# Performance work log

Measured on AMD Instinct MI355X. Metric: run time of the kernel, lower is better.

## Reference

```python
import jax, jax.numpy as jnp
import numpy as np

B, K, N, D = 16384, 32, 100000, 256


def setup_inputs() -> dict:
    key = jax.random.key(0)
    k1, k2 = jax.random.split(key)
    neigh_ids = jax.random.randint(k1, (B, K), 0, N)  # neighbor node ids per batch node
    features = jax.random.normal(k2, (N, D), dtype=jnp.float32)  # node feature/embedding table
    return {"neigh_ids": neigh_ids, "features": features}


def reference(neigh_ids, features):
    # Original builds a normalized [B, U] mask and does mask @ features[unique_ids];
    # that is exactly a mean over each row's neighbor features. We compute it
    # directly via gather + mean, honoring the sparse structure.
    gathered = features[neigh_ids]            # [B, K, D]
    to_feats = jnp.mean(gathered, axis=1)     # mean aggregation (mask.div(num_neigh) @ embed)
    return jax.nn.relu(to_feats)              # [B, D]
```

## Files before the change

### kernel.cpp

```cpp
#include <hip/hip_runtime.h>


constexpr int K  = 32;
constexpr int D  = 256;
constexpr int D4 = D / 4;

__global__ __launch_bounds__(256) void gnn_agg_kernel(
    const int* __restrict__ neigh_ids,
    const float* __restrict__ features,
    float* __restrict__ out,
    int n_rows)
{
    const int waves_per_block = blockDim.x >> 6;
    const int lane = threadIdx.x & 63;
    const int row_stride = gridDim.x * waves_per_block;

    const float4* __restrict__ f4 = reinterpret_cast<const float4*>(features);
    float4* __restrict__ o4 = reinterpret_cast<float4*>(out);

    for (int row = blockIdx.x * waves_per_block + (threadIdx.x >> 6);
         row < n_rows; row += row_stride) {

        const int4* __restrict__ idp =
            reinterpret_cast<const int4*>(neigh_ids + (size_t)row * K);
        int4 id8[K / 4];
        #pragma unroll
        for (int c = 0; c < K / 4; ++c) id8[c] = idp[c];

        float4 acc = make_float4(0.f, 0.f, 0.f, 0.f);
        #pragma unroll
        for (int c = 0; c < K / 4; ++c) {
            const float4 v0 = f4[(size_t)id8[c].x * D4 + lane];
            const float4 v1 = f4[(size_t)id8[c].y * D4 + lane];
            const float4 v2 = f4[(size_t)id8[c].z * D4 + lane];
            const float4 v3 = f4[(size_t)id8[c].w * D4 + lane];
            acc.x += v0.x + v1.x + v2.x + v3.x;
            acc.y += v0.y + v1.y + v2.y + v3.y;
            acc.z += v0.z + v1.z + v2.z + v3.z;
            acc.w += v0.w + v1.w + v2.w + v3.w;
        }

        const float s = 1.0f / (float)K;
        float4 r;
        r.x = fmaxf(acc.x * s, 0.f);
        r.y = fmaxf(acc.y * s, 0.f);
        r.z = fmaxf(acc.z * s, 0.f);
        r.w = fmaxf(acc.w * s, 0.f);

        o4[(size_t)row * D4 + lane] = r;
    }
}

extern "C" void kernel_launch(void* const* d_in, const int* in_sizes, int n_in,
                              void* d_out, int out_size, void* d_ws, size_t ws_size,
                              hipStream_t stream) {
    const int*   neigh_ids = (const int*)d_in[0];
    const float* features  = (const float*)d_in[1];
    float*       out       = (float*)d_out;

    const int n_rows = out_size / D;
    const int waves_per_block = 256 / 64;
    const int blocks = (n_rows + waves_per_block - 1) / waves_per_block;

    gnn_agg_kernel<<<blocks, 256, 0, stream>>>(neigh_ids, features, out, n_rows);
}
```

Measured before the change: 201.6 us.

## Stage neighbor feature rows into LDS via direct global-to-LDS loads with double buffering

Replaces direct register gathers of neighbor feature rows with global_load_lds DMA into per-wave double-buffered shared memory, 4 rows per chunk. The next chunk is issued before the current one is summed, with s_waitcnt vmcnt used to order the two. The aim is to keep loads in flight while the adds run. It adds LDS traffic and reads, and lowers outstanding parallelism compared with the original fully unrolled 32 independent loads. The manual waitcnt reasoning is also fragile (no LDS wait, and LDS writes and reads are not fenced).

```diff
diff --git a/kernel.cpp b/kernel.cpp
--- a/kernel.cpp
+++ b/kernel.cpp
@@ -4,6 +4,15 @@
 constexpr int K  = 32;
 constexpr int D  = 256;
 constexpr int D4 = D / 4;
+constexpr int CHUNK  = 4;
+constexpr int NCHUNK = K / CHUNK;
+
+#define AS1 __attribute__((address_space(1)))
+#define AS3 __attribute__((address_space(3)))
+
+__device__ __forceinline__ void dma_row_16B_per_lane(const float* gp, float* lp) {
+    __builtin_amdgcn_global_load_lds((const AS1 void*)gp, (AS3 void*)lp, 16, 0, 0);
+}
 
 __global__ __launch_bounds__(256) void gnn_agg_kernel(
     const int* __restrict__ neigh_ids,
@@ -11,33 +20,47 @@
     float* __restrict__ out,
     int n_rows)
 {
-    const int waves_per_block = blockDim.x >> 6;
+    __shared__ __align__(16) float smem[4][2][CHUNK][D];
+    const int w    = threadIdx.x >> 6;
     const int lane = threadIdx.x & 63;
-    const int row_stride = gridDim.x * waves_per_block;
 
     const float4* __restrict__ f4 = reinterpret_cast<const float4*>(features);
-    float4* __restrict__ o4 = reinterpret_cast<float4*>(out);
+    float4* __restrict__ o4       = reinterpret_cast<float4*>(out);
 
-    for (int row = blockIdx.x * waves_per_block + (threadIdx.x >> 6);
-         row < n_rows; row += row_stride) {
+    for (int row = (int)blockIdx.x * 4 + w; row < n_rows; row += (int)gridDim.x * 4) {
+        const int4* idp = reinterpret_cast<const int4*>(neigh_ids + (size_t)row * K);
+        int4 idq[NCHUNK];
+        #pragma unroll
+        for (int c = 0; c < NCHUNK; ++c) idq[c] = idp[c];
 
-        const int4* __restrict__ idp =
-            reinterpret_cast<const int4*>(neigh_ids + (size_t)row * K);
-        int4 id8[K / 4];
-        #pragma unroll
-        for (int c = 0; c < K / 4; ++c) id8[c] = idp[c];
+        {
+            const int4 q = idq[0];
+            dma_row_16B_per_lane((const float*)(f4 + (size_t)q.x * D4 + lane), &smem[w][0][0][0]);
+            dma_row_16B_per_lane((const float*)(f4 + (size_t)q.y * D4 + lane), &smem[w][0][1][0]);
+            dma_row_16B_per_lane((const float*)(f4 + (size_t)q.z * D4 + lane), &smem[w][0][2][0]);
+            dma_row_16B_per_lane((const float*)(f4 + (size_t)q.w * D4 + lane), &smem[w][0][3][0]);
+        }
 
         float4 acc = make_float4(0.f, 0.f, 0.f, 0.f);
         #pragma unroll
-        for (int c = 0; c < K / 4; ++c) {
-            const float4 v0 = f4[(size_t)id8[c].x * D4 + lane];
-            const float4 v1 = f4[(size_t)id8[c].y * D4 + lane];
-            const float4 v2 = f4[(size_t)id8[c].z * D4 + lane];
-            const float4 v3 = f4[(size_t)id8[c].w * D4 + lane];
-            acc.x += v0.x + v1.x + v2.x + v3.x;
-            acc.y += v0.y + v1.y + v2.y + v3.y;
-            acc.z += v0.z + v1.z + v2.z + v3.z;
-            acc.w += v0.w + v1.w + v2.w + v3.w;
+        for (int c = 0; c < NCHUNK; ++c) {
+            if (c + 1 < NCHUNK) {
+                const int4 q  = idq[c + 1];
+                const int b1  = (c + 1) & 1;
+                dma_row_16B_per_lane((const float*)(f4 + (size_t)q.x * D4 + lane), &smem[w][b1][0][0]);
+                dma_row_16B_per_lane((const float*)(f4 + (size_t)q.y * D4 + lane), &smem[w][b1][1][0]);
+                dma_row_16B_per_lane((const float*)(f4 + (size_t)q.z * D4 + lane), &smem[w][b1][2][0]);
+                dma_row_16B_per_lane((const float*)(f4 + (size_t)q.w * D4 + lane), &smem[w][b1][3][0]);
+                asm volatile("s_waitcnt vmcnt(4)" ::: "memory");
+            } else {
+                asm volatile("s_waitcnt vmcnt(0)" ::: "memory");
+            }
+            const int b = c & 1;
+            #pragma unroll
+            for (int k = 0; k < CHUNK; ++k) {
+                const float4 v = reinterpret_cast<const float4*>(&smem[w][b][k][0])[lane];
+                acc.x += v.x; acc.y += v.y; acc.z += v.z; acc.w += v.w;
+            }
         }
 
         const float s = 1.0f / (float)K;
@@ -46,7 +69,6 @@
         r.y = fmaxf(acc.y * s, 0.f);
         r.z = fmaxf(acc.z * s, 0.f);
         r.w = fmaxf(acc.w * s, 0.f);
-
         o4[(size_t)row * D4 + lane] = r;
     }
 }
@@ -59,8 +81,7 @@
     float*       out       = (float*)d_out;
 
     const int n_rows = out_size / D;
-    const int waves_per_block = 256 / 64;
-    const int blocks = (n_rows + waves_per_block - 1) / waves_per_block;
+    const int blocks = (n_rows + 3) / 4;
 
     gnn_agg_kernel<<<blocks, 256, 0, stream>>>(neigh_ids, features, out, n_rows);
 }
```

Result: no change. 201.4 us (-0.1%).
